# Kernel optimization log

Hardware: AMD Instinct MI355X
Metric: run time of the kernel (lower is better)

The kernel has to match this reference:

```python
import jax, jax.numpy as jnp
import numpy as np

N = 50000      # nodes
E = 400000     # directed edges (self-loops added inside reference, per PyG default)
DIN = 256
DH = 32
HEADS = 8
DOUT = 40
SLOPE = 0.2    # GATv2Conv negative_slope default


def _gatv2_layer(x, src, dst, Wl, bl, Wr, br, att, bias, heads, out_ch):
    """One GATv2Conv (concat=True). x:[n,din], src/dst:[e], att:[heads,out_ch]."""
    n = x.shape[0]
    xl = (x @ Wl + bl).reshape(n, heads, out_ch)   # source transform
    xr = (x @ Wr + br).reshape(n, heads, out_ch)   # target transform
    e = jax.nn.leaky_relu(xl[src] + xr[dst], SLOPE)          # [e, H, C]
    s = jnp.einsum('ehc,hc->eh', e, att)                     # per-edge attention logits
    smax = jax.ops.segment_max(s, dst, num_segments=n)       # stable softmax over in-edges
    ex = jnp.exp(s - smax[dst])
    denom = jax.ops.segment_sum(ex, dst, num_segments=n)
    alpha = ex / denom[dst]                                  # [e, H]
    out = jax.ops.segment_sum(alpha[:, :, None] * xl[src], dst, num_segments=n)
    return out.reshape(n, heads * out_ch) + bias


def setup_inputs() -> dict:
    key = jax.random.key(0)
    ks = jax.random.split(key, 8)
    def gl(k, shape, fan_in):
        return jax.random.normal(k, shape, jnp.float32) * np.float32(1.0 / np.sqrt(fan_in))
    return {
        'x': jax.random.normal(ks[0], (N, DIN), jnp.float32),
        'edge_index': jax.random.randint(ks[1], (2, E), 0, N, jnp.int32),
        'W1l': gl(ks[2], (DIN, HEADS * DH), DIN),
        'b1l': jnp.zeros((HEADS * DH,), jnp.float32),
        'W1r': gl(ks[3], (DIN, HEADS * DH), DIN),
        'b1r': jnp.zeros((HEADS * DH,), jnp.float32),
        'att1': gl(ks[4], (HEADS, DH), DH),
        'bias1': jnp.zeros((HEADS * DH,), jnp.float32),
        'W2l': gl(ks[5], (HEADS * DH, DOUT), HEADS * DH),
        'b2l': jnp.zeros((DOUT,), jnp.float32),
        'W2r': gl(ks[6], (HEADS * DH, DOUT), HEADS * DH),
        'b2r': jnp.zeros((DOUT,), jnp.float32),
        'att2': gl(ks[7], (1, DOUT), DOUT),
        'bias2': jnp.zeros((DOUT,), jnp.float32),
    }


def reference(x, edge_index, W1l, b1l, W1r, b1r, att1, bias1,
              W2l, b2l, W2r, b2r, att2, bias2):
    n = x.shape[0]
    loop = jnp.arange(n, dtype=edge_index.dtype)  # add_self_loops=True (PyG default)
    src = jnp.concatenate([edge_index[0], loop])
    dst = jnp.concatenate([edge_index[1], loop])
    # eval mode: F.dropout is identity; normalization='none' -> Identity
    h = _gatv2_layer(x, src, dst, W1l, b1l, W1r, b1r, att1, bias1, HEADS, DH)
    h = jax.nn.elu(h)
    out = _gatv2_layer(h, src, dst, W2l, b2l, W2r, b2r, att2, bias2, 1, DOUT)
    return jax.nn.log_softmax(out, axis=1)
```

## Files before the change

kernel.cpp:

```cpp
#include <hip/hip_runtime.h>
#include <math.h>

#define NODES 50000
#define NEDGE 400000
#define ETOT  450000
#define DIN   256
#define C1    256
#define C2    40
#define SCAN_NB ((NODES + 255) / 256)

typedef __attribute__((ext_vector_type(8))) short bfrag;
typedef __attribute__((ext_vector_type(4))) float facc;

#define GPTR(p) (const __attribute__((address_space(1))) unsigned int*)(p)
#define LPTR(p) (__attribute__((address_space(3))) unsigned int*)(p)

static __device__ __forceinline__ float bf2f(unsigned int u16) {
    unsigned int x = u16 << 16;
    float f;
    __builtin_memcpy(&f, &x, 4);
    return f;
}
static __device__ __forceinline__ float bitsf(unsigned int x) {
    float f;
    __builtin_memcpy(&f, &x, 4);
    return f;
}
static __device__ __forceinline__ unsigned short f2bf(float f) {
    unsigned int x;
    __builtin_memcpy(&x, &f, 4);
    unsigned int r = x + 0x7fffu + ((x >> 16) & 1u);
    return (unsigned short)(r >> 16);
}
static __device__ __forceinline__ float fexp2(float x) {
#if __has_builtin(__builtin_amdgcn_exp2f)
    return __builtin_amdgcn_exp2f(x);
#else
    return exp2f(x);
#endif
}

static __device__ __forceinline__ float2 pk_fma(float2 a, float2 b, float2 c) {
    float2 d;
    asm("v_pk_fma_f32 %0, %1, %2, %3" : "=v"(d) : "v"(a), "v"(b), "v"(c));
    return d;
}
static __device__ __forceinline__ float2 pk_add(float2 a, float2 b) {
    float2 d;
    asm("v_pk_add_f32 %0, %1, %2" : "=v"(d) : "v"(a), "v"(b));
    return d;
}
static __device__ __forceinline__ float2 pk_mul(float2 a, float2 b) {
    float2 d;
    asm("v_pk_mul_f32 %0, %1, %2" : "=v"(d) : "v"(a), "v"(b));
    return d;
}

__global__ __launch_bounds__(256)
void cvt_bf16(const float* __restrict__ in, unsigned short* __restrict__ out, int n8) {
    int i = blockIdx.x * 256 + threadIdx.x;
    if (i >= n8) return;
    const float4* p = (const float4*)in + (size_t)i * 2;
    float4 u0 = p[0], u1 = p[1];
    bfrag pk;
    pk[0] = (short)f2bf(u0.x); pk[1] = (short)f2bf(u0.y);
    pk[2] = (short)f2bf(u0.z); pk[3] = (short)f2bf(u0.w);
    pk[4] = (short)f2bf(u1.x); pk[5] = (short)f2bf(u1.y);
    pk[6] = (short)f2bf(u1.z); pk[7] = (short)f2bf(u1.w);
    *(bfrag*)(out + (size_t)i * 8) = pk;
}

__global__ void zero_int(int* p, int n) {
    int i = blockIdx.x * blockDim.x + threadIdx.x;
    if (i < n) p[i] = 0;
}

__global__ void count_kernel(const int* __restrict__ dstRow, int* __restrict__ cnt) {
    int e = blockIdx.x * blockDim.x + threadIdx.x;
    if (e >= ETOT) return;
    int d = (e < NEDGE) ? dstRow[e] : (e - NEDGE);
    atomicAdd(&cnt[d], 1);
}

__global__ __launch_bounds__(256)
void scan_blk(const int* __restrict__ cnt, int* __restrict__ off, int* __restrict__ blkTot) {
    __shared__ int buf[256];
    const int t = threadIdx.x;
    const int i = blockIdx.x * 256 + t;
    int v = (i < NODES) ? cnt[i] : 0;
    buf[t] = v;
    __syncthreads();
    #pragma unroll
    for (int d = 1; d < 256; d <<= 1) {
        int add = (t >= d) ? buf[t - d] : 0;
        __syncthreads();
        buf[t] += add;
        __syncthreads();
    }
    if (i < NODES) off[i] = buf[t] - v;
    if (t == 255) blkTot[blockIdx.x] = buf[255];
}

__global__ __launch_bounds__(256)
void scan_top(const int* __restrict__ blkTot, int* __restrict__ blkOff, int* __restrict__ offEnd) {
    __shared__ int buf[256];
    const int t = threadIdx.x;
    int v = (t < SCAN_NB) ? blkTot[t] : 0;
    buf[t] = v;
    __syncthreads();
    #pragma unroll
    for (int d = 1; d < 256; d <<= 1) {
        int add = (t >= d) ? buf[t - d] : 0;
        __syncthreads();
        buf[t] += add;
        __syncthreads();
    }
    if (t < SCAN_NB) blkOff[t] = buf[t] - v;
    if (t == 255) *offEnd = buf[255];
}

__global__ __launch_bounds__(256)
void scan_fix(int* __restrict__ off, int* __restrict__ wrk, const int* __restrict__ blkOff) {
    const int i = blockIdx.x * 256 + threadIdx.x;
    if (i < NODES) {
        int v = off[i] + blkOff[blockIdx.x];
        off[i] = v;
        wrk[i] = v;
    }
}

__global__ void place_kernel(const int* __restrict__ srcRow, const int* __restrict__ dstRow,
                             int* __restrict__ wrk, int* __restrict__ csr) {
    int e = blockIdx.x * blockDim.x + threadIdx.x;
    if (e >= ETOT) return;
    int d, s;
    if (e < NEDGE) { d = dstRow[e]; s = srcRow[e]; }
    else           { d = e - NEDGE; s = d; }
    int slot = atomicAdd(&wrk[d], 1);
    csr[slot] = s;
}

__global__ void prep_w(const float* __restrict__ Wl, const float* __restrict__ Wr,
                       unsigned short* __restrict__ Wt, int K, int Nhalf) {
    int idx = blockIdx.x * 256 + threadIdx.x;
    int n = idx / K;
    int k = idx - n * K;
    if (n >= 2 * Nhalf) return;
    float v = (n < Nhalf) ? Wl[(size_t)k * Nhalf + n] : Wr[(size_t)k * Nhalf + (n - Nhalf)];
    Wt[idx] = f2bf(v);
}

#define GBM 128
#define GBN 128
#define GBK 32

template<typename OUTT>
__global__ __launch_bounds__(256)
void mfma_gemm(const unsigned short* __restrict__ Ab, const unsigned short* __restrict__ Bt,
               const float* __restrict__ bl, const float* __restrict__ br,
               OUTT* __restrict__ Cl, OUTT* __restrict__ Cr,
               int M, int K, int Nrows, int Nhalf, int nbnShift)
{
    __shared__ __align__(16) unsigned short As[GBM * GBK];
    __shared__ __align__(16) unsigned short Bs[GBN * GBK];

    const int tid  = threadIdx.x;
    const int lane = tid & 63;
    const int w    = tid >> 6;
    const int wr   = w >> 1;
    const int wc   = w & 1;
    const int bx   = blockIdx.x >> nbnShift;
    const int by   = blockIdx.x & ((1 << nbnShift) - 1);
    const int row0 = bx * GBM;
    const int col0 = by * GBN;

    facc acc[4][4];
    #pragma unroll
    for (int i = 0; i < 4; ++i)
        #pragma unroll
        for (int j = 0; j < 4; ++j) {
            facc z = {0.f, 0.f, 0.f, 0.f};
            acc[i][j] = z;
        }

    const int rA  = lane >> 2;
    const int sA  = lane & 3;
    const int kgA = sA ^ ((rA >> 1) & 3);

    for (int k0 = 0; k0 < K; k0 += GBK) {
        if (k0) __syncthreads();

        #pragma unroll
        for (int p = 0; p < 2; ++p) {
            int chunk = p * 4 + w;
            int r_loc = chunk * 16 + rA;
            int grow  = row0 + r_loc;
            if (grow < M)
                __builtin_amdgcn_global_load_lds(
                    GPTR(Ab + (size_t)grow * K + k0 + kgA * 8),
                    LPTR(As + chunk * 512), 16, 0, 0);
        }
        #pragma unroll
        for (int p = 0; p < 2; ++p) {
            int chunk = p * 4 + w;
            int r_loc = chunk * 16 + rA;
            int grow  = col0 + r_loc;
            if (grow < Nrows)
                __builtin_amdgcn_global_load_lds(
                    GPTR(Bt + (size_t)grow * K + k0 + kgA * 8),
                    LPTR(Bs + chunk * 512), 16, 0, 0);
        }

        __syncthreads();

        const int fr    = lane & 15;
        const int sRead = (lane >> 4) ^ ((fr >> 1) & 3);
        bfrag af[4], bfv[4];
        #pragma unroll
        for (int mi = 0; mi < 4; ++mi)
            af[mi] = *(const bfrag*)(As + (wr * 64 + mi * 16 + fr) * 32 + sRead * 8);
        #pragma unroll
        for (int ni = 0; ni < 4; ++ni)
            bfv[ni] = *(const bfrag*)(Bs + (wc * 64 + ni * 16 + fr) * 32 + sRead * 8);
        #pragma unroll
        for (int mi = 0; mi < 4; ++mi)
            #pragma unroll
            for (int ni = 0; ni < 4; ++ni)
                acc[mi][ni] = __builtin_amdgcn_mfma_f32_16x16x32_bf16(
                    af[mi], bfv[ni], acc[mi][ni], 0, 0, 0);
    }

    #pragma unroll
    for (int mi = 0; mi < 4; ++mi) {
        const int rbase = row0 + wr * 64 + mi * 16 + ((lane >> 4) << 2);
        #pragma unroll
        for (int ni = 0; ni < 4; ++ni) {
            const int col = col0 + wc * 64 + ni * 16 + (lane & 15);
            #pragma unroll
            for (int rg = 0; rg < 4; ++rg) {
                int r = rbase + rg;
                if (r >= M) continue;
                float v = acc[mi][ni][rg];
                if (col < Nhalf) {
                    v += bl[col];
                    if constexpr (sizeof(OUTT) == 2)
                        Cl[(size_t)r * Nhalf + col] = (OUTT)f2bf(v);
                    else
                        Cl[(size_t)r * Nhalf + col] = (OUTT)v;
                } else if (col < 2 * Nhalf) {
                    int c2 = col - Nhalf;
                    v += br[c2];
                    if constexpr (sizeof(OUTT) == 2)
                        Cr[(size_t)r * Nhalf + c2] = (OUTT)f2bf(v);
                    else
                        Cr[(size_t)r * Nhalf + c2] = (OUTT)v;
                }
            }
        }
    }
}

__global__ __launch_bounds__(256)
void fused_l1(const int* __restrict__ off,
              const int* __restrict__ csr, const unsigned short* __restrict__ xl,
              const unsigned short* xr, const float* __restrict__ att,
              const float* __restrict__ bias, unsigned short* hout)
{
    const int lane = threadIdx.x & 63;
    const int n    = blockIdx.x * 4 + (threadIdx.x >> 6);
    if (n >= NODES) return;

    const int a = off[n], b = off[n + 1];

    const uint2 xrn = *(const uint2*)(xr + (size_t)n * C1 + lane * 4);
    const float2 xr01 = {bitsf(xrn.x << 16), bitsf(xrn.x & 0xffff0000u)};
    const float2 xr23 = {bitsf(xrn.y << 16), bitsf(xrn.y & 0xffff0000u)};
    const float4 wv = *(const float4*)(att + lane * 4);
    const float L2E = 1.4426950408889634f;
    const float2 w6_01 = {wv.x * (0.6f * L2E), wv.y * (0.6f * L2E)};
    const float2 w4_01 = {wv.x * (0.4f * L2E), wv.y * (0.4f * L2E)};
    const float2 w6_23 = {wv.z * (0.6f * L2E), wv.w * (0.6f * L2E)};
    const float2 w4_23 = {wv.z * (0.4f * L2E), wv.w * (0.4f * L2E)};

    float m = -INFINITY, d = 0.f;
    float2 ac01 = {0.f, 0.f}, ac23 = {0.f, 0.f};

    for (int base = a; base < b; base += 64) {
        const int cn = min(64, b - base);
        int mySrc = 0;
        if (lane < cn) mySrc = csr[base + lane];

        #define ROW1(i) (*(const uint2*)(xl + (size_t)__shfl(mySrc, min((i), cn - 1)) * C1 + lane * 4))
        #define PROC1(i, R)                                                          \
        {                                                                            \
            const float2 x01 = {bitsf((R).x << 16), bitsf((R).x & 0xffff0000u)};     \
            const float2 x23 = {bitsf((R).y << 16), bitsf((R).y & 0xffff0000u)};     \
            const float2 v01 = pk_add(x01, xr01);                                    \
            const float2 v23 = pk_add(x23, xr23);                                    \
            const float2 av01 = {fabsf(v01.x), fabsf(v01.y)};                        \
            const float2 av23 = {fabsf(v23.x), fabsf(v23.y)};                        \
            float2 p2 = pk_mul(w6_01, v01);                                          \
            p2 = pk_fma(w4_01, av01, p2);                                            \
            p2 = pk_fma(w6_23, v23, p2);                                             \
            p2 = pk_fma(w4_23, av23, p2);                                            \
            float p = p2.x + p2.y;                                                   \
            p += __shfl_xor(p, 1);                                                   \
            p += __shfl_xor(p, 2);                                                   \
            p += __shfl_xor(p, 4);                                                   \
            if (__any(p > m + 8.f)) {                                                \
                const float mN = fmaxf(m, p);                                        \
                const float sc = fexp2(m - mN);                                      \
                const float wg = fexp2(p - mN);                                      \
                m = mN;                                                              \
                d = d * sc + wg;                                                     \
                const float2 s2 = {sc, sc};                                          \
                const float2 g2 = {wg, wg};                                          \
                ac01 = pk_fma(g2, x01, pk_mul(ac01, s2));                            \
                ac23 = pk_fma(g2, x23, pk_mul(ac23, s2));                            \
            } else {                                                                 \
                const float wg = fexp2(p - m);                                       \
                d += wg;                                                             \
                const float2 g2 = {wg, wg};                                          \
                ac01 = pk_fma(g2, x01, ac01);                                        \
                ac23 = pk_fma(g2, x23, ac23);                                        \
            }                                                                        \
        }

        uint2 r0, r1, r2, r3;
        r0 = ROW1(0);
        if (1 < cn) r1 = ROW1(1);
        if (2 < cn) r2 = ROW1(2);
        if (3 < cn) r3 = ROW1(3);
        for (int i = 0; i < cn; i += 4) {
            PROC1(i, r0);
            if (i + 4 < cn) r0 = ROW1(i + 4);
            if (i + 1 < cn) {
                PROC1(i + 1, r1);
                if (i + 5 < cn) r1 = ROW1(i + 5);
            }
            if (i + 2 < cn) {
                PROC1(i + 2, r2);
                if (i + 6 < cn) r2 = ROW1(i + 6);
            }
            if (i + 3 < cn) {
                PROC1(i + 3, r3);
                if (i + 7 < cn) r3 = ROW1(i + 7);
            }
        }
        #undef ROW1
        #undef PROC1
    }

    const float inv = 1.f / d;
    const float4 bv = *(const float4*)(bias + lane * 4);
    float v0 = ac01.x * inv + bv.x, v1 = ac01.y * inv + bv.y;
    float v2 = ac23.x * inv + bv.z, v3 = ac23.y * inv + bv.w;
    v0 = v0 > 0.f ? v0 : (expf(v0) - 1.f);
    v1 = v1 > 0.f ? v1 : (expf(v1) - 1.f);
    v2 = v2 > 0.f ? v2 : (expf(v2) - 1.f);
    v3 = v3 > 0.f ? v3 : (expf(v3) - 1.f);
    uint2 o;
    o.x = (unsigned int)f2bf(v0) | ((unsigned int)f2bf(v1) << 16);
    o.y = (unsigned int)f2bf(v2) | ((unsigned int)f2bf(v3) << 16);
    *(uint2*)(hout + (size_t)n * C1 + lane * 4) = o;
}

__global__ __launch_bounds__(256)
void fused_l2(const int* __restrict__ off,
              const int* __restrict__ csr, const float* __restrict__ h2l,
              const float* __restrict__ h2r, const float* __restrict__ att,
              const float* __restrict__ bias, float* __restrict__ out)
{
    const int lane = threadIdx.x & 63;
    const int n    = blockIdx.x * 4 + (threadIdx.x >> 6);
    if (n >= NODES) return;
    const int l8 = lane & 7;
    const int g  = lane >> 3;

    const int a = off[n], b = off[n + 1];
    const float L2E = 1.4426950408889634f;

    float w6[5], w4[5], xr[5];
    #pragma unroll
    for (int j = 0; j < 5; ++j) {
        const int c = l8 + 8 * j;
        const float w = att[c];
        w6[j] = w * (0.6f * L2E);
        w4[j] = w * (0.4f * L2E);
        xr[j] = h2r[(size_t)n * C2 + c];
    }

    float m = -INFINITY, dl = 0.f;
    float acc[5] = {0.f, 0.f, 0.f, 0.f, 0.f};

    for (int base = a; base < b; base += 64) {
        const int cn = min(64, b - base);
        int mySrc = 0;
        if (lane < cn) mySrc = csr[base + lane];

        for (int c0 = 0; c0 < cn; c0 += 8) {
            const int idx = c0 + g;
            const bool active = idx < cn;
            const int src = __shfl(mySrc, min(idx, cn - 1));
            const float* row = h2l + (size_t)src * C2 + l8;
            float R[5];
            #pragma unroll
            for (int j = 0; j < 5; ++j) R[j] = row[8 * j];

            float p = 0.f;
            #pragma unroll
            for (int j = 0; j < 5; ++j) {
                const float v = R[j] + xr[j];
                p = fmaf(w6[j], v, p);
                p = fmaf(w4[j], fabsf(v), p);
            }
            p += __shfl_xor(p, 1);
            p += __shfl_xor(p, 2);
            p += __shfl_xor(p, 4);
            if (!active) p = -INFINITY;

            if (__any(p > m + 8.f)) {
                float pm = p;
                pm = fmaxf(pm, __shfl_xor(pm, 8));
                pm = fmaxf(pm, __shfl_xor(pm, 16));
                pm = fmaxf(pm, __shfl_xor(pm, 32));
                const float mN = fmaxf(m, pm);
                const float sc = fexp2(m - mN);
                const float wg = fexp2(p - mN);
                m = mN;
                dl = dl * sc + wg;
                #pragma unroll
                for (int j = 0; j < 5; ++j) acc[j] = fmaf(wg, R[j], acc[j] * sc);
            } else {
                const float wg = fexp2(p - m);
                dl += wg;
                #pragma unroll
                for (int j = 0; j < 5; ++j) acc[j] = fmaf(wg, R[j], acc[j]);
            }
        }
    }

    #pragma unroll
    for (int o = 8; o < 64; o <<= 1) {
        dl += __shfl_xor(dl, o);
        #pragma unroll
        for (int j = 0; j < 5; ++j) acc[j] += __shfl_xor(acc[j], o);
    }

    const float inv = 1.f / dl;
    float v[5];
    float mx = -INFINITY;
    #pragma unroll
    for (int j = 0; j < 5; ++j) {
        v[j] = acc[j] * inv + bias[l8 + 8 * j];
        mx = fmaxf(mx, v[j]);
    }
    mx = fmaxf(mx, __shfl_xor(mx, 1));
    mx = fmaxf(mx, __shfl_xor(mx, 2));
    mx = fmaxf(mx, __shfl_xor(mx, 4));
    float s = 0.f;
    #pragma unroll
    for (int j = 0; j < 5; ++j) s += expf(v[j] - mx);
    s += __shfl_xor(s, 1);
    s += __shfl_xor(s, 2);
    s += __shfl_xor(s, 4);
    const float lg = logf(s);
    if (g == 0) {
        #pragma unroll
        for (int j = 0; j < 5; ++j)
            out[(size_t)n * C2 + l8 + 8 * j] = v[j] - mx - lg;
    }
}

extern "C" void kernel_launch(void* const* d_in, const int* in_sizes, int n_in,
                              void* d_out, int out_size, void* d_ws, size_t ws_size,
                              hipStream_t stream)
{
    const float* x     = (const float*)d_in[0];
    const int*   ei    = (const int*)  d_in[1];
    const float* W1l   = (const float*)d_in[2];
    const float* b1l   = (const float*)d_in[3];
    const float* W1r   = (const float*)d_in[4];
    const float* b1r   = (const float*)d_in[5];
    const float* att1  = (const float*)d_in[6];
    const float* bias1 = (const float*)d_in[7];
    const float* W2l   = (const float*)d_in[8];
    const float* b2l   = (const float*)d_in[9];
    const float* W2r   = (const float*)d_in[10];
    const float* b2r   = (const float*)d_in[11];
    const float* att2  = (const float*)d_in[12];
    const float* bias2 = (const float*)d_in[13];
    float* out = (float*)d_out;

    float* ws = (float*)d_ws;
    unsigned short* xl1 = (unsigned short*)ws;
    unsigned short* xr1 = (unsigned short*)(ws + 6400000);
    unsigned short* xb  = (unsigned short*)(ws + 12800000);
    int*   csr    = (int*)(ws + 19200000);
    int*   off    = csr + ETOT;
    int*   cnt    = off + (NODES + 1);
    int*   wrk    = cnt + NODES;
    int*   blkTot = wrk + NODES;
    int*   blkOff = blkTot + SCAN_NB;
    unsigned short* Wt1 = (unsigned short*)(ws + 19810000);
    unsigned short* Wt2 = (unsigned short*)(ws + 19880000);
    unsigned short* h = xr1;
    float* h2l = ws;
    float* h2r = ws + 2000000;

    const int* srcRow = ei;
    const int* dstRow = ei + NEDGE;

    zero_int<<<(NODES + 255) / 256, 256, 0, stream>>>(cnt, NODES);
    count_kernel<<<(ETOT + 255) / 256, 256, 0, stream>>>(dstRow, cnt);
    scan_blk<<<SCAN_NB, 256, 0, stream>>>(cnt, off, blkTot);
    scan_top<<<1, 256, 0, stream>>>(blkTot, blkOff, off + NODES);
    scan_fix<<<SCAN_NB, 256, 0, stream>>>(off, wrk, blkOff);
    place_kernel<<<(ETOT + 255) / 256, 256, 0, stream>>>(srcRow, dstRow, wrk, csr);

    cvt_bf16<<<(NODES * DIN / 8 + 255) / 256, 256, 0, stream>>>(x, xb, NODES * DIN / 8);
    prep_w<<<(512 * 256 + 255) / 256, 256, 0, stream>>>(W1l, W1r, Wt1, DIN, C1);
    prep_w<<<(80 * 256 + 255) / 256, 256, 0, stream>>>(W2l, W2r, Wt2, C1, C2);

    mfma_gemm<unsigned short><<<((NODES + GBM - 1) / GBM) * 4, 256, 0, stream>>>(
        xb, Wt1, b1l, b1r, xl1, xr1, NODES, DIN, 2 * C1, C1, 2);
    fused_l1<<<(NODES + 3) / 4, 256, 0, stream>>>(off, csr, xl1, xr1, att1, bias1, h);

    mfma_gemm<float><<<(NODES + GBM - 1) / GBM, 256, 0, stream>>>(
        h, Wt2, b2l, b2r, h2l, h2r, NODES, C1, 2 * C2, C2, 0);
    fused_l2<<<(NODES + 3) / 4, 256, 0, stream>>>(off, csr, h2l, h2r, att2, bias2, out);
}
```

Baseline: 221.6 us.

## Double-buffer GEMM LDS tiles and add XCD-aware block swizzle

New measurement: 215.3 us. -2.9%, faster.

```diff
diff --git a/kernel.cpp b/kernel.cpp
--- a/kernel.cpp
+++ b/kernel.cpp
@@ -154,23 +154,34 @@
 #define GBN 128
 #define GBK 32
 
-template<typename OUTT>
+template<typename OUTT, bool SWZ>
 __global__ __launch_bounds__(256)
 void mfma_gemm(const unsigned short* __restrict__ Ab, const unsigned short* __restrict__ Bt,
                const float* __restrict__ bl, const float* __restrict__ br,
                OUTT* __restrict__ Cl, OUTT* __restrict__ Cr,
                int M, int K, int Nrows, int Nhalf, int nbnShift)
 {
-    __shared__ __align__(16) unsigned short As[GBM * GBK];
-    __shared__ __align__(16) unsigned short Bs[GBN * GBK];
+    __shared__ __align__(16) unsigned short As[2][GBM * GBK];
+    __shared__ __align__(16) unsigned short Bs[2][GBN * GBK];
 
     const int tid  = threadIdx.x;
     const int lane = tid & 63;
     const int w    = tid >> 6;
     const int wr   = w >> 1;
     const int wc   = w & 1;
-    const int bx   = blockIdx.x >> nbnShift;
-    const int by   = blockIdx.x & ((1 << nbnShift) - 1);
+
+    int tile;
+    if constexpr (SWZ) {
+        const int nwg = gridDim.x;
+        const int q = nwg >> 3, r = nwg & 7;
+        const int xcd = blockIdx.x & 7;
+        const int idx = blockIdx.x >> 3;
+        tile = (xcd < r ? xcd * (q + 1) : r * (q + 1) + (xcd - r) * q) + idx;
+    } else {
+        tile = blockIdx.x;
+    }
+    const int bx   = tile >> nbnShift;
+    const int by   = tile & ((1 << nbnShift) - 1);
     const int row0 = bx * GBM;
     const int col0 = by * GBN;
 
@@ -184,51 +195,58 @@
         }
 
     const int rA  = lane >> 2;
-    const int sA  = lane & 3;
-    const int kgA = sA ^ ((rA >> 1) & 3);
-
-    for (int k0 = 0; k0 < K; k0 += GBK) {
-        if (k0) __syncthreads();
-
-        #pragma unroll
-        for (int p = 0; p < 2; ++p) {
-            int chunk = p * 4 + w;
-            int r_loc = chunk * 16 + rA;
-            int grow  = row0 + r_loc;
-            if (grow < M)
-                __builtin_amdgcn_global_load_lds(
-                    GPTR(Ab + (size_t)grow * K + k0 + kgA * 8),
-                    LPTR(As + chunk * 512), 16, 0, 0);
+    const int kgA = (lane & 3) ^ ((rA >> 1) & 3);
+
+    #define STAGE(bufi, k0)                                                     \
+    {                                                                           \
+        _Pragma("unroll")                                                       \
+        for (int p = 0; p < 2; ++p) {                                           \
+            const int chunk = p * 4 + w;                                        \
+            const int r_loc = chunk * 16 + rA;                                  \
+            const int ga = min(row0 + r_loc, M - 1);                            \
+            __builtin_amdgcn_global_load_lds(                                   \
+                GPTR(Ab + (size_t)ga * K + (k0) + kgA * 8),                     \
+                LPTR(&As[bufi][chunk * 512]), 16, 0, 0);                        \
+            const int gb = min(col0 + r_loc, Nrows - 1);                        \
+            __builtin_amdgcn_global_load_lds(                                   \
+                GPTR(Bt + (size_t)gb * K + (k0) + kgA * 8),                     \
+                LPTR(&Bs[bufi][chunk * 512]), 16, 0, 0);                        \
+        }                                                                       \
+    }
+
+    const int fr    = lane & 15;
+    const int sRead = (lane >> 4) ^ ((fr >> 1) & 3);
+    const int nt    = K / GBK;
+
+    STAGE(0, 0);
+    for (int t = 0; t < nt; ++t) {
+        const int cur = t & 1;
+        if (t + 1 < nt) {
+            STAGE(cur ^ 1, (t + 1) * GBK);
+            asm volatile("s_waitcnt vmcnt(4)" ::: "memory");
+        } else {
+            asm volatile("s_waitcnt vmcnt(0)" ::: "memory");
         }
-        #pragma unroll
-        for (int p = 0; p < 2; ++p) {
-            int chunk = p * 4 + w;
-            int r_loc = chunk * 16 + rA;
-            int grow  = col0 + r_loc;
-            if (grow < Nrows)
-                __builtin_amdgcn_global_load_lds(
-                    GPTR(Bt + (size_t)grow * K + k0 + kgA * 8),
-                    LPTR(Bs + chunk * 512), 16, 0, 0);
-        }
-
-        __syncthreads();
-
-        const int fr    = lane & 15;
-        const int sRead = (lane >> 4) ^ ((fr >> 1) & 3);
+        __builtin_amdgcn_s_barrier();
+        __builtin_amdgcn_sched_barrier(0);
+
         bfrag af[4], bfv[4];
         #pragma unroll
         for (int mi = 0; mi < 4; ++mi)
-            af[mi] = *(const bfrag*)(As + (wr * 64 + mi * 16 + fr) * 32 + sRead * 8);
+            af[mi] = *(const bfrag*)(&As[cur][(wr * 64 + mi * 16 + fr) * 32 + sRead * 8]);
         #pragma unroll
         for (int ni = 0; ni < 4; ++ni)
-            bfv[ni] = *(const bfrag*)(Bs + (wc * 64 + ni * 16 + fr) * 32 + sRead * 8);
+            bfv[ni] = *(const bfrag*)(&Bs[cur][(wc * 64 + ni * 16 + fr) * 32 + sRead * 8]);
         #pragma unroll
         for (int mi = 0; mi < 4; ++mi)
             #pragma unroll
             for (int ni = 0; ni < 4; ++ni)
                 acc[mi][ni] = __builtin_amdgcn_mfma_f32_16x16x32_bf16(
                     af[mi], bfv[ni], acc[mi][ni], 0, 0, 0);
-    }
+
+        __builtin_amdgcn_s_barrier();
+    }
+    #undef STAGE
 
     #pragma unroll
     for (int mi = 0; mi < 4; ++mi) {
@@ -522,11 +540,11 @@
     prep_w<<<(512 * 256 + 255) / 256, 256, 0, stream>>>(W1l, W1r, Wt1, DIN, C1);
     prep_w<<<(80 * 256 + 255) / 256, 256, 0, stream>>>(W2l, W2r, Wt2, C1, C2);
 
-    mfma_gemm<unsigned short><<<((NODES + GBM - 1) / GBM) * 4, 256, 0, stream>>>(
+    mfma_gemm<unsigned short, true><<<((NODES + GBM - 1) / GBM) * 4, 256, 0, stream>>>(
         xb, Wt1, b1l, b1r, xl1, xr1, NODES, DIN, 2 * C1, C1, 2);
     fused_l1<<<(NODES + 3) / 4, 256, 0, stream>>>(off, csr, xl1, xr1, att1, bias1, h);
 
-    mfma_gemm<float><<<(NODES + GBM - 1) / GBM, 256, 0, stream>>>(
+    mfma_gemm<float, false><<<(NODES + GBM - 1) / GBM, 256, 0, stream>>>(
         h, Wt2, b2l, b2r, h2l, h2r, NODES, C1, 2 * C2, C2, 0);
     fused_l2<<<(NODES + 3) / 4, 256, 0, stream>>>(off, csr, h2l, h2r, att2, bias2, out);
 }
```
